# Kernel tuning notes

Hardware: AMD Instinct MI355X
Metric: run time of the kernel (lower is better)

Reference implementation:

```python
import jax, jax.numpy as jnp
import numpy as np

D_EMBED = 1024
D_QUERY = 512
NEG_INF = -1.0e9  # matches masked_fill value in the torch module


def setup_inputs() -> dict:
    key = jax.random.key(0)
    k_x, k_q, k_k, k_v, k_m = jax.random.split(key, 5)
    B, T = 8, 2048
    x = jax.random.normal(k_x, (B, T, D_EMBED), dtype=jnp.float32)
    # nn.Linear(d_embed, d_query, bias=False): y = x @ W^T; store W as (d_embed, d_query)
    sc = 1.0 / np.sqrt(D_EMBED)
    Wq = jax.random.normal(k_q, (D_EMBED, D_QUERY), dtype=jnp.float32) * sc
    Wk = jax.random.normal(k_k, (D_EMBED, D_QUERY), dtype=jnp.float32) * sc
    Wv = jax.random.normal(k_v, (D_EMBED, D_QUERY), dtype=jnp.float32) * sc
    attn_mask = jax.random.randint(k_m, (B, T), 0, 2).astype(jnp.bool_)
    return {"x": x, "Wq": Wq, "Wk": Wk, "Wv": Wv, "attn_mask": attn_mask}


def reference(x, Wq, Wk, Wv, attn_mask):
    # x: (B, T, d_embed)
    q = jnp.einsum("btd,dq->btq", x, Wq)  # (B, T, d_query)
    k = jnp.einsum("btd,dq->btq", x, Wk)
    v = jnp.einsum("btd,dq->btq", x, Wv)
    # NOTE: original module applies NO 1/sqrt(d) scaling.
    logits = jnp.einsum("btq,bsq->bts", q, k)  # (B, T, T)
    # attn_mask (B, T) broadcasts over the query axis: mask keys where mask is False
    logits = jnp.where(attn_mask[..., None, :], logits, NEG_INF)
    A = jax.nn.softmax(logits, axis=-1)
    return jnp.einsum("bts,bsq->btq", A, v)  # (B, T, d_query)
```

## Files before the change

### kernel.cpp

```cpp
#include <hip/hip_runtime.h>
#include <hip/hip_bf16.h>
#include <cstddef>
#include <cstdint>

#define BATCH 8
#define SEQ   2048
#define DEMB  1024
#define DQ    512

typedef __attribute__((ext_vector_type(8))) _Float16 f16x8;
typedef __attribute__((ext_vector_type(4))) float f32x4;

#define MFMA16(a, b, c) __builtin_amdgcn_mfma_f32_16x16x32_f16((a), (b), (c), 0, 0, 0)

#define GLDS16(gp, lp) __builtin_amdgcn_global_load_lds(                      \
    (const __attribute__((address_space(1))) void*)(gp),                      \
    (__attribute__((address_space(3))) void*)(lp), 16, 0, 0)

#define VM_BAR(N)                                                             \
  asm volatile("s_waitcnt vmcnt(" #N ")\n\ts_barrier" ::: "memory")
#define VM_LGKM_BAR(N)                                                        \
  asm volatile("s_waitcnt vmcnt(" #N ") lgkmcnt(0)\n\ts_barrier" ::: "memory")

__global__ __launch_bounds__(256) void mprep(
    const int* __restrict__ maskg, int* __restrict__ pidx,
    int* __restrict__ cnt)
{
  const int b = blockIdx.x;
  const int tid = threadIdx.x;
  __shared__ int tsum[256];
  int mv[8], s = 0;
  #pragma unroll
  for (int j = 0; j < 8; j++) {
    mv[j] = maskg[b * SEQ + tid * 8 + j];
    s += mv[j];
  }
  tsum[tid] = s;
  __syncthreads();
  for (int d = 1; d < 256; d <<= 1) {
    int v = (tid >= d) ? tsum[tid - d] : 0;
    __syncthreads();
    tsum[tid] += v;
    __syncthreads();
  }
  if (tid == 255) cnt[b] = tsum[255];
  int run = tsum[tid] - s;
  #pragma unroll
  for (int j = 0; j < 8; j++) {
    pidx[b * SEQ + tid * 8 + j] = mv[j] ? run : -1;
    run += mv[j];
  }
}

__global__ __launch_bounds__(256) void xprep(
    const float* __restrict__ x, _Float16* __restrict__ xh)
{
  size_t i = ((size_t)blockIdx.x * 256 + threadIdx.x) * 8;
  float4 a = *(const float4*)&x[i];
  float4 b = *(const float4*)&x[i + 4];
  f16x8 h;
  h[0] = (_Float16)a.x; h[1] = (_Float16)a.y;
  h[2] = (_Float16)a.z; h[3] = (_Float16)a.w;
  h[4] = (_Float16)b.x; h[5] = (_Float16)b.y;
  h[6] = (_Float16)b.z; h[7] = (_Float16)b.w;
  *(f16x8*)&xh[i] = h;
}

__global__ __launch_bounds__(256) void wprep(
    const float* __restrict__ Wq, const float* __restrict__ Wk,
    const float* __restrict__ Wv, _Float16* __restrict__ wt)
{
  int qidx = blockIdx.x * 256 + threadIdx.x;
  int w   = qidx >> 17;
  int rem = qidx & 131071;
  int k   = rem >> 7;
  int n   = (rem & 127) * 4;
  const float* W = (w == 0) ? Wq : (w == 1) ? Wk : Wv;
  float4 v = *(const float4*)&W[(size_t)k * DQ + n];
  _Float16* dst = wt + (size_t)w * (DQ * DEMB);
  dst[(size_t)(n + 0) * DEMB + k] = (_Float16)v.x;
  dst[(size_t)(n + 1) * DEMB + k] = (_Float16)v.y;
  dst[(size_t)(n + 2) * DEMB + k] = (_Float16)v.z;
  dst[(size_t)(n + 3) * DEMB + k] = (_Float16)v.w;
}

__global__ __launch_bounds__(256) void proj_f16(
    const _Float16* __restrict__ xh, const _Float16* __restrict__ wt,
    const int* __restrict__ pidx,
    _Float16* __restrict__ kf, _Float16* __restrict__ vt,
    _Float16* __restrict__ qpack)
{
  const int w  = blockIdx.z;
  const int mt = blockIdx.y, nt = blockIdx.x;

  __shared__ _Float16 Xs[128][40];
  __shared__ _Float16 Ws[128][40];

  const int tid  = threadIdx.x;
  const int wave = tid >> 6, l = tid & 63;
  const int wm = wave >> 1, wn = wave & 1;
  const int lo4 = l & 15, hi2 = l >> 4;

  f32x4 acc[4][4];
  #pragma unroll
  for (int mf = 0; mf < 4; mf++)
    #pragma unroll
    for (int nf = 0; nf < 4; nf++)
      #pragma unroll
      for (int i = 0; i < 4; i++) acc[mf][nf][i] = 0.f;

  const int    srow  = tid >> 1;
  const int    skh   = (tid & 1) * 16;
  const size_t xbase = (size_t)(mt * 128 + srow) * DEMB + skh;
  const size_t wbase = (size_t)w * (DQ * DEMB) + (size_t)(nt * 128 + srow) * DEMB + skh;

  #pragma unroll 1
  for (int k0 = 0; k0 < DEMB; k0 += 32) {
    *(f16x8*)&Xs[srow][skh]     = *(const f16x8*)&xh[xbase + k0];
    *(f16x8*)&Xs[srow][skh + 8] = *(const f16x8*)&xh[xbase + k0 + 8];
    *(f16x8*)&Ws[srow][skh]     = *(const f16x8*)&wt[wbase + k0];
    *(f16x8*)&Ws[srow][skh + 8] = *(const f16x8*)&wt[wbase + k0 + 8];
    __syncthreads();

    f16x8 a[4], bfr[4];
    #pragma unroll
    for (int mf = 0; mf < 4; mf++)
      a[mf] = *(const f16x8*)&Xs[wm*64 + mf*16 + lo4][hi2*8];
    #pragma unroll
    for (int nf = 0; nf < 4; nf++)
      bfr[nf] = *(const f16x8*)&Ws[wn*64 + nf*16 + lo4][hi2*8];
    #pragma unroll
    for (int mf = 0; mf < 4; mf++)
      #pragma unroll
      for (int nf = 0; nf < 4; nf++)
        acc[mf][nf] = MFMA16(a[mf], bfr[nf], acc[mf][nf]);
    __syncthreads();
  }

  const int mb = mt * 128 + wm * 64;
  const int nb = nt * 128 + wn * 64;
  #pragma unroll
  for (int mf = 0; mf < 4; mf++)
    #pragma unroll
    for (int nf = 0; nf < 4; nf++)
      #pragma unroll
      for (int i = 0; i < 4; i++) {
        int m = mb + mf*16 + hi2*4 + i;
        int n = nb + nf*16 + lo4;
        float val = acc[mf][nf][i];
        if (w == 0) {
          _Float16 h  = (_Float16)val;
          _Float16 lo = (_Float16)(val - (float)h);
          size_t base = (size_t)(m >> 6) * 65536 + (size_t)(m & 63) * 512 + n;
          qpack[base]         = h;
          qpack[base + 32768] = lo;
        } else if (w == 1) {
          int d_ = pidx[m];
          if (d_ >= 0)
            kf[((size_t)((m >> 11) << 11) + d_) * 512 + n] = (_Float16)val;
        } else {
          int d_ = pidx[m];
          if (d_ >= 0)
            vt[(size_t)(m >> 11) * (512 * 2048) + (size_t)n * 2048 + d_]
                = (_Float16)val;
        }
      }
}

__global__ __launch_bounds__(512, 2) void flash_v4(
    const _Float16* __restrict__ kfp, const _Float16* __restrict__ vtp,
    const int* __restrict__ cntg,
    float* dout)
{
  const int bb = blockIdx.x & 7;
  const int qt = blockIdx.x >> 3;
  const int q0 = qt * 64;

  const int tid = threadIdx.x;
  const int w = tid >> 6, l = tid & 63;
  const int qw = w & 3;
  const int kw = w >> 2;
  const int lo4 = l & 15, hi2 = l >> 4;

  __shared__ _Float16 Kst[2][64][256];
  __shared__ _Float16 Vst[2][256][64];
  __shared__ _Float16 P[64 * 64];
  __shared__ float pmax[2][64], psum[2][64];

  const _Float16* qpk = (const _Float16*)dout + (size_t)(bb * 32 + qt) * 65536;
  const char*     kb  = (const char*)(kfp + (size_t)bb * SEQ * 512);
  const char*     vtb = (const char*)(vtp + (size_t)bb * (512 * 2048));

  const _Float16* qhi = qpk + (size_t)(qw * 16 + lo4) * 512;
  const _Float16* qlo = qhi + 32768;

  const int cnt = cntg[bb];
  const int nkt = (cnt + 63) >> 6;

#define STAGE_K(KT, H, B) do {                                                \
    const char* kg_ = kb + (size_t)(KT) * 64 * 1024;                          \
    char* lb_ = (char*)&Kst[(B)][0][0];                                       \
    _Pragma("unroll")                                                         \
    for (int i_ = 0; i_ < 4; i_++) {                                          \
      int D_ = i_ * 8192 + tid * 16;                                          \
      int row_ = D_ >> 9, cb_ = D_ & 511;                                     \
      GLDS16(kg_ + (size_t)row_ * 1024 + (H) * 512 +                          \
                 (cb_ ^ ((row_ & 7) << 4)),                                   \
             lb_ + D_);                                                       \
    } } while (0)

#define STAGE_V(KT, H, B) do {                                                \
    const char* vg_ = vtb + (size_t)(KT) * 128;                               \
    char* lb_ = (char*)&Vst[(B)][0][0];                                       \
    _Pragma("unroll")                                                         \
    for (int i_ = 0; i_ < 4; i_++) {                                          \
      int D_ = i_ * 8192 + tid * 16;                                          \
      int row_ = D_ >> 7, cb_ = D_ & 127;                                     \
      GLDS16(vg_ + (size_t)((H) * 256 + row_) * 4096 +                        \
                 (cb_ ^ ((row_ & 7) << 4)),                                   \
             lb_ + D_);                                                       \
    } } while (0)

#define QK_HALF(H, B) do {                                                    \
    const char* kl_ = (const char*)&Kst[(B)][0][0];                           \
    const int r0_ = kw * 32 + lo4, r1_ = r0_ + 16;                            \
    const int sw_ = (lo4 & 7) << 4;                                           \
    _Pragma("unroll")                                                         \
    for (int s_ = 0; s_ < 8; s_++) {                                          \
      const int dby_ = (s_ * 32 + hi2 * 8) * 2;                               \
      f16x8 k0 = *(const f16x8*)(kl_ + r0_ * 512 + (dby_ ^ sw_));             \
      f16x8 k1 = *(const f16x8*)(kl_ + r1_ * 512 + (dby_ ^ sw_));             \
      __builtin_amdgcn_s_setprio(1);                                          \
      S[0] = MFMA16(fq[(H) * 8 + s_], k0, S[0]);                              \
      S[1] = MFMA16(fq[(H) * 8 + s_], k1, S[1]);                              \
      S[0] = MFMA16(fql[(H) * 8 + s_], k0, S[0]);                             \
      S[1] = MFMA16(fql[(H) * 8 + s_], k1, S[1]);                             \
      __builtin_amdgcn_s_setprio(0);                                          \
    } } while (0)

#define PV_HALF(H, B) do {                                                    \
    const char* vl_ = (const char*)&Vst[(B)][0][0];                           \
    _Pragma("unroll")                                                         \
    for (int j_ = 0; j_ < 8; j_++) {                                          \
      const int dl_ = j_ * 32 + kw * 16 + lo4;                                \
      const int vs_ = (dl_ & 7) << 4;                                         \
      f16x8 v0 = *(const f16x8*)(vl_ + dl_ * 128 + ((hi2 * 16) ^ vs_));       \
      f16x8 v1 = *(const f16x8*)(vl_ + dl_ * 128 + ((64 + hi2 * 16) ^ vs_));  \
      __builtin_amdgcn_s_setprio(1);                                          \
      o[(H) * 8 + j_] = MFMA16(pa[0], v0, o[(H) * 8 + j_]);                   \
      o[(H) * 8 + j_] = MFMA16(pa[1], v1, o[(H) * 8 + j_]);                   \
      __builtin_amdgcn_s_setprio(0);                                          \
    } } while (0)

  f16x8 fq[16], fql[16];
  #pragma unroll
  for (int st = 0; st < 16; st++) {
    fq[st]  = *(const f16x8*)(qhi + st * 32 + hi2 * 8);
    fql[st] = *(const f16x8*)(qlo + st * 32 + hi2 * 8);
  }
  STAGE_K(0, 0, 0);
  __syncthreads();

  f32x4 o[16];
  #pragma unroll
  for (int f = 0; f < 16; f++)
    #pragma unroll
    for (int i = 0; i < 4; i++) o[f][i] = 0.f;

  float m_run[4], l_run[4], m_runP = -3.0e38f;
  #pragma unroll
  for (int i = 0; i < 4; i++) { m_run[i] = -3.0e38f; l_run[i] = 0.f; }

  const int ki0 = kw * 32 + lo4;
  const int ki1 = ki0 + 16;

  #pragma unroll 1
  for (int kt = 0; kt < nkt; kt++) {
    const int key0 = kt * 64;

    STAGE_K(kt, 1, 1);
    STAGE_V(kt, 0, 0);
    VM_BAR(8);

    f32x4 S[2];
    #pragma unroll
    for (int f = 0; f < 2; f++)
      #pragma unroll
      for (int i = 0; i < 4; i++) S[f][i] = 0.f;
    QK_HALF(0, 0);

    VM_BAR(4);
    QK_HALF(1, 1);

    STAGE_V(kt, 1, 1);
    STAGE_K(kt + 1, 0, 0);

    const bool t0 = (key0 + ki0 >= cnt);
    const bool t1 = (key0 + ki1 >= cnt);
    #pragma unroll
    for (int i = 0; i < 4; i++) {
      if (t0) S[0][i] = -1.0e9f;
      if (t1) S[1][i] = -1.0e9f;
      float mx = fmaxf(S[0][i], S[1][i]);
      #pragma unroll
      for (int off = 1; off < 16; off <<= 1)
        mx = fmaxf(mx, __shfl_xor(mx, off, 64));
      float p0 = __expf(S[0][i] - mx);
      float p1 = __expf(S[1][i] - mx);
      int row = qw*16 + hi2*4 + i;
      int swz = (row & 7) << 4;
      int b0  = (row*128 + (kw*32 + lo4)*2) ^ swz;
      int b1  = (row*128 + (kw*32 + 16 + lo4)*2) ^ swz;
      *(_Float16*)((char*)P + b0) = (_Float16)p0;
      *(_Float16*)((char*)P + b1) = (_Float16)p1;
      float ps = p0 + p1;
      #pragma unroll
      for (int off = 1; off < 16; off <<= 1) ps += __shfl_xor(ps, off, 64);
      if (lo4 == 0) { pmax[kw][row] = mx; psum[kw][row] = ps; }
    }

    VM_LGKM_BAR(8);

    float oscale[4];
    #pragma unroll
    for (int i = 0; i < 4; i++) {
      int row = qw*16 + hi2*4 + i;
      float m0 = pmax[0][row], m1 = pmax[1][row];
      float s0 = psum[0][row], s1 = psum[1][row];
      float mn = fmaxf(m_run[i], fmaxf(m0, m1));
      oscale[i] = __expf(m_run[i] - mn);
      l_run[i] = l_run[i] * oscale[i]
               + __expf(m0 - mn) * s0 + __expf(m1 - mn) * s1;
      m_run[i] = mn;
    }
    #pragma unroll
    for (int f = 0; f < 16; f++)
      #pragma unroll
      for (int i = 0; i < 4; i++) o[f][i] *= oscale[i];

    f16x8 pa[2];
    {
      const int prow = qw*16 + lo4;
      float m0p = pmax[0][prow], m1p = pmax[1][prow];
      float mnp = fmaxf(m_runP, fmaxf(m0p, m1p));
      m_runP = mnp;
      _Float16 c0 = (_Float16)__expf(m0p - mnp);
      _Float16 c1 = (_Float16)__expf(m1p - mnp);
      const int psw = (prow & 7) << 4;
      pa[0] = *(const f16x8*)((const char*)P + prow*128 + ((hi2*16) ^ psw));
      pa[1] = *(const f16x8*)((const char*)P + prow*128 + ((64 + hi2*16) ^ psw));
      pa[0] = pa[0] * c0;
      pa[1] = pa[1] * c1;
    }

    PV_HALF(0, 0);
    VM_BAR(4);
    PV_HALF(1, 1);
  }
#undef STAGE_K
#undef STAGE_V
#undef QK_HALF
#undef PV_HALF

  asm volatile("s_waitcnt vmcnt(0)" ::: "memory");

  #pragma unroll
  for (int i = 0; i < 4; i++) {
    float inv = 1.0f / l_run[i];
    int rowg = bb * SEQ + q0 + qw*16 + hi2*4 + i;
    #pragma unroll
    for (int h = 0; h < 2; h++)
      #pragma unroll
      for (int j = 0; j < 8; j++) {
        int d = h*256 + j*32 + kw*16 + lo4;
        dout[(size_t)rowg * 512 + d] = o[h*8 + j][i] * inv;
      }
  }
}

extern "C" void kernel_launch(void* const* d_in, const int* in_sizes, int n_in,
                              void* d_out, int out_size, void* d_ws, size_t ws_size,
                              hipStream_t stream)
{
  const float* x    = (const float*)d_in[0];
  const float* Wq   = (const float*)d_in[1];
  const float* Wk   = (const float*)d_in[2];
  const float* Wv   = (const float*)d_in[3];
  const int*   mask = (const int*)d_in[4];

  _Float16* wsh = (_Float16*)d_ws;
  _Float16* KF = wsh;
  _Float16* VT = wsh +  8388608;
  _Float16* WT = wsh + 16777216;
  _Float16* XH = wsh + 18350080;
  int* PIDX    = (int*)(wsh + 35127296);
  int* CNT     = PIDX + 16384;

  mprep<<<BATCH, 256, 0, stream>>>(mask, PIDX, CNT);
  xprep<<<8192, 256, 0, stream>>>(x, XH);
  wprep<<<1536, 256, 0, stream>>>(Wq, Wk, Wv, WT);

  dim3 pgrid(4, 128, 3);
  proj_f16<<<pgrid, 256, 0, stream>>>(XH, WT, PIDX, KF, VT, (_Float16*)d_out);

  flash_v4<<<256, 512, 0, stream>>>(KF, VT, CNT, (float*)d_out);
}
```

Before: 274.7 us.

## Merge prep kernels into one launch and widen projection tile to 128x256

Fuses the mask prefix-sum, x fp16 conversion and weight transpose kernels into a single launch that dispatches on block index, which removes two kernel launches and the gaps between them. The projection GEMM now uses 512 threads (8 waves) per block and a 128x256 output tile, so each X tile loaded into LDS is reused across twice as many output columns. The cost is more LDS per block and fewer blocks in the grid (768 instead of 1536), which may lower occupancy.

```diff
diff --git a/kernel.cpp b/kernel.cpp
--- a/kernel.cpp
+++ b/kernel.cpp
@@ -22,69 +22,67 @@
 #define VM_LGKM_BAR(N)                                                        \
   asm volatile("s_waitcnt vmcnt(" #N ") lgkmcnt(0)\n\ts_barrier" ::: "memory")
 
-__global__ __launch_bounds__(256) void mprep(
+__global__ __launch_bounds__(256) void prep_all(
+    const float* __restrict__ x, _Float16* __restrict__ xh,
+    const float* __restrict__ Wq, const float* __restrict__ Wk,
+    const float* __restrict__ Wv, _Float16* __restrict__ wt,
     const int* __restrict__ maskg, int* __restrict__ pidx,
     int* __restrict__ cnt)
 {
-  const int b = blockIdx.x;
+  const int bid = blockIdx.x;
   const int tid = threadIdx.x;
-  __shared__ int tsum[256];
-  int mv[8], s = 0;
-  #pragma unroll
-  for (int j = 0; j < 8; j++) {
-    mv[j] = maskg[b * SEQ + tid * 8 + j];
-    s += mv[j];
-  }
-  tsum[tid] = s;
-  __syncthreads();
-  for (int d = 1; d < 256; d <<= 1) {
-    int v = (tid >= d) ? tsum[tid - d] : 0;
+
+  if (bid < 8192) {
+    size_t i = ((size_t)bid * 256 + tid) * 8;
+    float4 a = *(const float4*)&x[i];
+    float4 b = *(const float4*)&x[i + 4];
+    f16x8 h;
+    h[0] = (_Float16)a.x; h[1] = (_Float16)a.y;
+    h[2] = (_Float16)a.z; h[3] = (_Float16)a.w;
+    h[4] = (_Float16)b.x; h[5] = (_Float16)b.y;
+    h[6] = (_Float16)b.z; h[7] = (_Float16)b.w;
+    *(f16x8*)&xh[i] = h;
+  } else if (bid < 9728) {
+    int qidx = (bid - 8192) * 256 + tid;
+    int w   = qidx >> 17;
+    int rem = qidx & 131071;
+    int k   = rem >> 7;
+    int n   = (rem & 127) * 4;
+    const float* W = (w == 0) ? Wq : (w == 1) ? Wk : Wv;
+    float4 v = *(const float4*)&W[(size_t)k * DQ + n];
+    _Float16* dst = wt + (size_t)w * (DQ * DEMB);
+    dst[(size_t)(n + 0) * DEMB + k] = (_Float16)v.x;
+    dst[(size_t)(n + 1) * DEMB + k] = (_Float16)v.y;
+    dst[(size_t)(n + 2) * DEMB + k] = (_Float16)v.z;
+    dst[(size_t)(n + 3) * DEMB + k] = (_Float16)v.w;
+  } else {
+    const int b = bid - 9728;
+    __shared__ int tsum[256];
+    int mv[8], s = 0;
+    #pragma unroll
+    for (int j = 0; j < 8; j++) {
+      mv[j] = maskg[b * SEQ + tid * 8 + j];
+      s += mv[j];
+    }
+    tsum[tid] = s;
     __syncthreads();
-    tsum[tid] += v;
-    __syncthreads();
-  }
-  if (tid == 255) cnt[b] = tsum[255];
-  int run = tsum[tid] - s;
-  #pragma unroll
-  for (int j = 0; j < 8; j++) {
-    pidx[b * SEQ + tid * 8 + j] = mv[j] ? run : -1;
-    run += mv[j];
+    for (int d = 1; d < 256; d <<= 1) {
+      int v = (tid >= d) ? tsum[tid - d] : 0;
+      __syncthreads();
+      tsum[tid] += v;
+      __syncthreads();
+    }
+    if (tid == 255) cnt[b] = tsum[255];
+    int run = tsum[tid] - s;
+    #pragma unroll
+    for (int j = 0; j < 8; j++) {
+      pidx[b * SEQ + tid * 8 + j] = mv[j] ? run : -1;
+      run += mv[j];
+    }
   }
 }
 
-__global__ __launch_bounds__(256) void xprep(
-    const float* __restrict__ x, _Float16* __restrict__ xh)
-{
-  size_t i = ((size_t)blockIdx.x * 256 + threadIdx.x) * 8;
-  float4 a = *(const float4*)&x[i];
-  float4 b = *(const float4*)&x[i + 4];
-  f16x8 h;
-  h[0] = (_Float16)a.x; h[1] = (_Float16)a.y;
-  h[2] = (_Float16)a.z; h[3] = (_Float16)a.w;
-  h[4] = (_Float16)b.x; h[5] = (_Float16)b.y;
-  h[6] = (_Float16)b.z; h[7] = (_Float16)b.w;
-  *(f16x8*)&xh[i] = h;
-}
-
-__global__ __launch_bounds__(256) void wprep(
-    const float* __restrict__ Wq, const float* __restrict__ Wk,
-    const float* __restrict__ Wv, _Float16* __restrict__ wt)
-{
-  int qidx = blockIdx.x * 256 + threadIdx.x;
-  int w   = qidx >> 17;
-  int rem = qidx & 131071;
-  int k   = rem >> 7;
-  int n   = (rem & 127) * 4;
-  const float* W = (w == 0) ? Wq : (w == 1) ? Wk : Wv;
-  float4 v = *(const float4*)&W[(size_t)k * DQ + n];
-  _Float16* dst = wt + (size_t)w * (DQ * DEMB);
-  dst[(size_t)(n + 0) * DEMB + k] = (_Float16)v.x;
-  dst[(size_t)(n + 1) * DEMB + k] = (_Float16)v.y;
-  dst[(size_t)(n + 2) * DEMB + k] = (_Float16)v.z;
-  dst[(size_t)(n + 3) * DEMB + k] = (_Float16)v.w;
-}
-
-__global__ __launch_bounds__(256) void proj_f16(
+__global__ __launch_bounds__(512) void proj_f16(
     const _Float16* __restrict__ xh, const _Float16* __restrict__ wt,
     const int* __restrict__ pidx,
     _Float16* __restrict__ kf, _Float16* __restrict__ vt,
@@ -94,11 +92,12 @@
   const int mt = blockIdx.y, nt = blockIdx.x;
 
   __shared__ _Float16 Xs[128][40];
-  __shared__ _Float16 Ws[128][40];
+  __shared__ _Float16 Ws[256][40];
 
   const int tid  = threadIdx.x;
   const int wave = tid >> 6, l = tid & 63;
-  const int wm = wave >> 1, wn = wave & 1;
+  const int wm = wave >> 2;
+  const int wn = wave & 3;
   const int lo4 = l & 15, hi2 = l >> 4;
 
   f32x4 acc[4][4];
@@ -109,17 +108,19 @@
       #pragma unroll
       for (int i = 0; i < 4; i++) acc[mf][nf][i] = 0.f;
 
-  const int    srow  = tid >> 1;
-  const int    skh   = (tid & 1) * 16;
-  const size_t xbase = (size_t)(mt * 128 + srow) * DEMB + skh;
-  const size_t wbase = (size_t)w * (DQ * DEMB) + (size_t)(nt * 128 + srow) * DEMB + skh;
+  const int    xsrow = tid >> 2;
+  const int    xskh  = (tid & 3) * 8;
+  const size_t xbase = (size_t)(mt * 128 + xsrow) * DEMB + xskh;
+  const int    wsrow = tid >> 1;
+  const int    wskh  = (tid & 1) * 16;
+  const size_t wbase = (size_t)w * (DQ * DEMB)
+                     + (size_t)(nt * 256 + wsrow) * DEMB + wskh;
 
   #pragma unroll 1
   for (int k0 = 0; k0 < DEMB; k0 += 32) {
-    *(f16x8*)&Xs[srow][skh]     = *(const f16x8*)&xh[xbase + k0];
-    *(f16x8*)&Xs[srow][skh + 8] = *(const f16x8*)&xh[xbase + k0 + 8];
-    *(f16x8*)&Ws[srow][skh]     = *(const f16x8*)&wt[wbase + k0];
-    *(f16x8*)&Ws[srow][skh + 8] = *(const f16x8*)&wt[wbase + k0 + 8];
+    *(f16x8*)&Xs[xsrow][xskh]    = *(const f16x8*)&xh[xbase + k0];
+    *(f16x8*)&Ws[wsrow][wskh]    = *(const f16x8*)&wt[wbase + k0];
+    *(f16x8*)&Ws[wsrow][wskh+8]  = *(const f16x8*)&wt[wbase + k0 + 8];
     __syncthreads();
 
     f16x8 a[4], bfr[4];
@@ -138,7 +139,7 @@
   }
 
   const int mb = mt * 128 + wm * 64;
-  const int nb = nt * 128 + wn * 64;
+  const int nb = nt * 256 + wn * 64;
   #pragma unroll
   for (int mf = 0; mf < 4; mf++)
     #pragma unroll
@@ -396,12 +397,10 @@
   int* PIDX    = (int*)(wsh + 35127296);
   int* CNT     = PIDX + 16384;
 
-  mprep<<<BATCH, 256, 0, stream>>>(mask, PIDX, CNT);
-  xprep<<<8192, 256, 0, stream>>>(x, XH);
-  wprep<<<1536, 256, 0, stream>>>(Wq, Wk, Wv, WT);
-
-  dim3 pgrid(4, 128, 3);
-  proj_f16<<<pgrid, 256, 0, stream>>>(XH, WT, PIDX, KF, VT, (_Float16*)d_out);
+  prep_all<<<9736, 256, 0, stream>>>(x, XH, Wq, Wk, Wv, WT, mask, PIDX, CNT);
+
+  dim3 pgrid(2, 128, 3);
+  proj_f16<<<pgrid, 512, 0, stream>>>(XH, WT, PIDX, KF, VT, (_Float16*)d_out);
 
   flash_v4<<<256, 512, 0, stream>>>(KF, VT, CNT, (float*)d_out);
 }
```

Result: faster. 256.3 us (-6.7%).
